# Performance work log

Measured on AMD Instinct MI355X. Metric: run time of the kernel, lower is better.

Reference implementation:

```python
import jax, jax.numpy as jnp
import numpy as np

D_MODEL = 1024
D_FF = 4096
N_EXPERTS = 8
TOP_K = 2
B, S = 4, 2048


def setup_inputs() -> dict:
    key = jax.random.key(0)
    ks = jax.random.split(key, 6)
    x = jax.random.normal(ks[0], (B, S, D_MODEL), dtype=jnp.float32)
    # router gate: nn.Linear(d_model, num_experts, bias=False), weight [E, D]
    gate_w = jax.random.normal(ks[1], (N_EXPERTS, D_MODEL), dtype=jnp.float32) * 0.01
    # expert MLPs, xavier-uniform init
    lim1 = float(np.sqrt(6.0 / (D_MODEL + D_FF)))
    W1 = jax.random.uniform(ks[2], (N_EXPERTS, D_FF, D_MODEL), minval=-lim1, maxval=lim1, dtype=jnp.float32)
    b1 = jnp.zeros((N_EXPERTS, D_FF), dtype=jnp.float32)
    W2 = jax.random.uniform(ks[3], (N_EXPERTS, D_MODEL, D_FF), minval=-lim1, maxval=lim1, dtype=jnp.float32)
    b2 = jnp.zeros((N_EXPERTS, D_MODEL), dtype=jnp.float32)
    return {"x": x, "gate_w": gate_w, "W1": W1, "b1": b1, "W2": W2, "b2": b2}


def reference(x, gate_w, W1, b1, W2, b2):
    Bb, Ss, D = x.shape
    xt = x.reshape(-1, D)                                  # [N, D]
    # --- router ---
    logits = xt @ gate_w.T                                 # [N, E]
    probs = jax.nn.softmax(logits, axis=-1)
    w_topk, idx = jax.lax.top_k(probs, TOP_K)              # [N, K]
    w_topk = w_topk / (jnp.sum(w_topk, axis=-1, keepdims=True) + 1e-9)
    # dense combine weights: zero for unselected experts    [N, E]
    comb = jnp.sum(jax.nn.one_hot(idx, N_EXPERTS, dtype=xt.dtype) * w_topk[..., None], axis=1)
    # --- experts (dense grouped GEMM over all experts) ---
    h = jnp.einsum('nd,efd->enf', xt, W1) + b1[:, None, :]  # [E, N, ff]
    h = jax.nn.relu(h)                                      # dropout=identity (eval)
    y = jnp.einsum('enf,edf->end', h, W2) + b2[:, None, :]  # [E, N, D]
    # --- weighted scatter/combine ---
    out = jnp.einsum('ne,end->nd', comb, y)                 # [N, D]
    return out.reshape(Bb, Ss, D)
```

## Files before the change

kernel.cpp:

```cpp
#include <hip/hip_runtime.h>
#include <hip/hip_bf16.h>
#include <stdint.h>

#define D_MODEL 1024
#define D_FF    4096
#define N_EXP   8
#define TOPK    2
#define NTOK    8192
#define NASSIGN (NTOK*TOPK)

#define BM 128
#define BN 128
#define BK 64
#define THREADS 256

typedef __bf16 bf16_t;
typedef __attribute__((ext_vector_type(8))) bf16_t bf16x8;
typedef __attribute__((ext_vector_type(4))) float f32x4;

__device__ __forceinline__ unsigned short f2bf(float f) {
    bf16_t b = (bf16_t)f;
    return __builtin_bit_cast(unsigned short, b);
}

__device__ __forceinline__ void gload_lds16(const void* g, void* l) {
    __builtin_amdgcn_global_load_lds(
        (const __attribute__((address_space(1))) void*)g,
        (__attribute__((address_space(3))) void*)l, 16, 0, 0);
}

__global__ void cvt_both_kernel(const float* __restrict__ W1, unsigned short* __restrict__ o1, int n1,
                                const float* __restrict__ W2, unsigned short* __restrict__ o2, int n2) {
    int stride = gridDim.x * blockDim.x;
    int q1 = n1 / 4, q2 = n2 / 4;
    for (int i = blockIdx.x * blockDim.x + threadIdx.x; i < q1 + q2; i += stride) {
        const float4* src; ushort4* dst; int k;
        if (i < q1) { src = (const float4*)W1; dst = (ushort4*)o1; k = i; }
        else        { src = (const float4*)W2; dst = (ushort4*)o2; k = i - q1; }
        float4 v = src[k];
        ushort4 o;
        o.x = f2bf(v.x); o.y = f2bf(v.y); o.z = f2bf(v.z); o.w = f2bf(v.w);
        dst[k] = o;
    }
}

__global__ __launch_bounds__(64) void router_kernel(
        const float* __restrict__ x, const float* __restrict__ gw,
        int* __restrict__ counts, int* __restrict__ ltok, float* __restrict__ lw,
        unsigned short* __restrict__ xb) {
    int n = blockIdx.x;
    int lane = threadIdx.x;
    const float* xr = x + (size_t)n * D_MODEL;
    unsigned short* xbr = xb + (size_t)n * D_MODEL;
    float acc[N_EXP];
    #pragma unroll
    for (int e = 0; e < N_EXP; e++) acc[e] = 0.f;
    #pragma unroll
    for (int i = 0; i < 4; i++) {
        int j = lane + i * 64;
        float4 v = ((const float4*)xr)[j];
        ushort4 o;
        o.x = f2bf(v.x); o.y = f2bf(v.y); o.z = f2bf(v.z); o.w = f2bf(v.w);
        ((ushort4*)xbr)[j] = o;
        int d = j * 4;
        #pragma unroll
        for (int e = 0; e < N_EXP; e++) {
            const float* g = gw + e * D_MODEL + d;
            acc[e] += v.x * g[0] + v.y * g[1] + v.z * g[2] + v.w * g[3];
        }
    }
    #pragma unroll
    for (int e = 0; e < N_EXP; e++) {
        #pragma unroll
        for (int off = 32; off > 0; off >>= 1)
            acc[e] += __shfl_down(acc[e], off);
    }
    if (lane == 0) {
        float mx = acc[0];
        #pragma unroll
        for (int e = 1; e < N_EXP; e++) mx = fmaxf(mx, acc[e]);
        float p[N_EXP];
        float s = 0.f;
        #pragma unroll
        for (int e = 0; e < N_EXP; e++) { p[e] = expf(acc[e] - mx); s += p[e]; }
        float inv = 1.f / s;
        #pragma unroll
        for (int e = 0; e < N_EXP; e++) p[e] *= inv;
        int i0 = 0;
        #pragma unroll
        for (int e = 1; e < N_EXP; e++) if (p[e] > p[i0]) i0 = e;
        int i1 = (i0 == 0) ? 1 : 0;
        #pragma unroll
        for (int e = 0; e < N_EXP; e++) if (e != i0 && p[e] > p[i1]) i1 = e;
        float s2 = p[i0] + p[i1] + 1e-9f;
        float w0 = p[i0] / s2, w1 = p[i1] / s2;
        int pos0 = atomicAdd(&counts[i0], 1);
        ltok[i0 * NTOK + pos0] = n; lw[i0 * NTOK + pos0] = w0;
        int pos1 = atomicAdd(&counts[i1], 1);
        ltok[i1 * NTOK + pos1] = n; lw[i1 * NTOK + pos1] = w1;
    }
}

__global__ void scan_kernel(const int* __restrict__ counts, int* __restrict__ offs) {
    if (threadIdx.x == 0 && blockIdx.x == 0) {
        int s = 0;
        for (int e = 0; e < N_EXP; e++) { offs[e] = s; s += counts[e]; }
    }
}


__global__ __launch_bounds__(THREADS, 3) void gemm1_kernel(
        const unsigned short* __restrict__ xb, const unsigned short* __restrict__ w1b,
        const float* __restrict__ b1,
        const int* __restrict__ counts, const int* __restrict__ offs,
        const int* __restrict__ ltok,
        unsigned short* __restrict__ hb) {
    const int NTM = NTOK / BM;
    int b = blockIdx.x;
    int e = b & 7;
    int idx = b >> 3;
    int nt = idx / NTM;
    int mt = idx % NTM;
    int cnt = counts[e];
    if (mt * BM >= cnt) return;

    __shared__ __align__(16) unsigned short As[BM * BK];
    __shared__ __align__(16) unsigned short Bs[BN * BK];

    int t = threadIdx.x;
    int lane = t & 63, w = t >> 6;
    int wr = w >> 1, wc = w & 1;

    int srow = t >> 3;
    int schunk = (t & 7) ^ (srow & 7);
    const unsigned short* aptr[4];
    const unsigned short* bptr[4];
    #pragma unroll
    for (int j = 0; j < 4; j++) {
        int rr = srow + j * 32;
        int slot = mt * BM + rr;
        int cs = slot < cnt ? slot : (cnt - 1);
        int tok = ltok[e * NTOK + cs];
        aptr[j] = xb + (size_t)tok * D_MODEL + schunk * 8;
        bptr[j] = w1b + ((size_t)e * D_FF + nt * BN + rr) * D_MODEL + schunk * 8;
    }
    char* As_b = (char*)As;
    char* Bs_b = (char*)Bs;

    int arow_base = wr * 64 + (lane & 15);
    int brow_base = wc * 64 + (lane & 15);
    int ch[2];
    #pragma unroll
    for (int ks = 0; ks < 2; ks++)
        ch[ks] = ((ks * 4 + (lane >> 4)) ^ (lane & 7)) << 4;

    f32x4 acc[4][4];
    #pragma unroll
    for (int m = 0; m < 4; m++)
        #pragma unroll
        for (int n = 0; n < 4; n++)
            acc[m][n] = (f32x4){0.f, 0.f, 0.f, 0.f};

    for (int k0 = 0; k0 < D_MODEL; k0 += BK) {
        #pragma unroll
        for (int j = 0; j < 4; j++) {
            gload_lds16(aptr[j] + k0, As_b + j * 4096 + t * 16);
            gload_lds16(bptr[j] + k0, Bs_b + j * 4096 + t * 16);
        }
        __syncthreads();
        bf16x8 af[2][4], bf[2][4];
        #pragma unroll
        for (int ks = 0; ks < 2; ks++) {
            #pragma unroll
            for (int m = 0; m < 4; m++)
                af[ks][m] = *(const bf16x8*)(As_b + (size_t)(arow_base + m * 16) * 128 + ch[ks]);
            #pragma unroll
            for (int n = 0; n < 4; n++)
                bf[ks][n] = *(const bf16x8*)(Bs_b + (size_t)(brow_base + n * 16) * 128 + ch[ks]);
        }
        #pragma unroll
        for (int ks = 0; ks < 2; ks++)
            #pragma unroll
            for (int m = 0; m < 4; m++)
                #pragma unroll
                for (int n = 0; n < 4; n++)
                    acc[m][n] = __builtin_amdgcn_mfma_f32_16x16x32_bf16(af[ks][m], bf[ks][n], acc[m][n], 0, 0, 0);
        __syncthreads();
    }

    int hbase = offs[e];
    float biasv[4];
    #pragma unroll
    for (int n = 0; n < 4; ++n)
        biasv[n] = b1[e * D_FF + nt * BN + wc * 64 + n * 16 + (lane & 15)];
    #pragma unroll
    for (int m = 0; m < 4; ++m) {
        int s0 = mt * BM + wr * 64 + m * 16 + (lane >> 4) * 4;
        #pragma unroll
        for (int rq = 0; rq < 4; ++rq) {
            int s = s0 + rq;
            if (s < cnt) {
                size_t rowoff = (size_t)(hbase + s) * D_FF + nt * BN + wc * 64 + (lane & 15);
                #pragma unroll
                for (int n = 0; n < 4; ++n) {
                    float v = fmaxf(acc[m][n][rq] + biasv[n], 0.f);
                    hb[rowoff + n * 16] = f2bf(v);
                }
            }
        }
    }
}

__global__ __launch_bounds__(THREADS, 3) void gemm2_kernel(
        const unsigned short* __restrict__ hb, const unsigned short* __restrict__ w2b,
        const float* __restrict__ b2,
        const int* __restrict__ counts, const int* __restrict__ offs,
        const int* __restrict__ ltok, const float* __restrict__ lw,
        float* __restrict__ out) {
    const int NTM = NTOK / BM;
    int b = blockIdx.x;
    int e = b & 7;
    int idx = b >> 3;
    int nt = idx / NTM;
    int mt = idx % NTM;
    int cnt = counts[e];
    if (mt * BM >= cnt) return;
    int hbase = offs[e];

    __shared__ __align__(16) unsigned short As[BM * BK];
    __shared__ __align__(16) unsigned short Bs[BN * BK];

    int t = threadIdx.x;
    int lane = t & 63, w = t >> 6;
    int wr = w >> 1, wc = w & 1;

    int srow = t >> 3;
    int schunk = (t & 7) ^ (srow & 7);
    const unsigned short* aptr[4];
    const unsigned short* bptr[4];
    #pragma unroll
    for (int j = 0; j < 4; j++) {
        int rr = srow + j * 32;
        int slot = mt * BM + rr;
        int cs = slot < cnt ? slot : (cnt - 1);
        aptr[j] = hb + (size_t)(hbase + cs) * D_FF + schunk * 8;
        bptr[j] = w2b + ((size_t)e * D_MODEL + nt * BN + rr) * D_FF + schunk * 8;
    }
    char* As_b = (char*)As;
    char* Bs_b = (char*)Bs;

    int arow_base = wr * 64 + (lane & 15);
    int brow_base = wc * 64 + (lane & 15);
    int ch[2];
    #pragma unroll
    for (int ks = 0; ks < 2; ks++)
        ch[ks] = ((ks * 4 + (lane >> 4)) ^ (lane & 7)) << 4;

    f32x4 acc[4][4];
    #pragma unroll
    for (int m = 0; m < 4; m++)
        #pragma unroll
        for (int n = 0; n < 4; n++)
            acc[m][n] = (f32x4){0.f, 0.f, 0.f, 0.f};

    for (int k0 = 0; k0 < D_FF; k0 += BK) {
        #pragma unroll
        for (int j = 0; j < 4; j++) {
            gload_lds16(aptr[j] + k0, As_b + j * 4096 + t * 16);
            gload_lds16(bptr[j] + k0, Bs_b + j * 4096 + t * 16);
        }
        __syncthreads();
        bf16x8 af[2][4], bf[2][4];
        #pragma unroll
        for (int ks = 0; ks < 2; ks++) {
            #pragma unroll
            for (int m = 0; m < 4; m++)
                af[ks][m] = *(const bf16x8*)(As_b + (size_t)(arow_base + m * 16) * 128 + ch[ks]);
            #pragma unroll
            for (int n = 0; n < 4; n++)
                bf[ks][n] = *(const bf16x8*)(Bs_b + (size_t)(brow_base + n * 16) * 128 + ch[ks]);
        }
        #pragma unroll
        for (int ks = 0; ks < 2; ks++)
            #pragma unroll
            for (int m = 0; m < 4; m++)
                #pragma unroll
                for (int n = 0; n < 4; n++)
                    acc[m][n] = __builtin_amdgcn_mfma_f32_16x16x32_bf16(af[ks][m], bf[ks][n], acc[m][n], 0, 0, 0);
        __syncthreads();
    }

    int lbase = e * NTOK;
    float biasv[4];
    #pragma unroll
    for (int n = 0; n < 4; ++n)
        biasv[n] = b2[e * D_MODEL + nt * BN + wc * 64 + n * 16 + (lane & 15)];
    #pragma unroll
    for (int m = 0; m < 4; ++m) {
        int s0 = mt * BM + wr * 64 + m * 16 + (lane >> 4) * 4;
        #pragma unroll
        for (int rq = 0; rq < 4; ++rq) {
            int s = s0 + rq;
            if (s >= cnt) continue;
            int tok = ltok[lbase + s];
            float wgt = lw[lbase + s];
            float* orow = out + (size_t)tok * D_MODEL + nt * BN + wc * 64 + (lane & 15);
            #pragma unroll
            for (int n = 0; n < 4; ++n)
                atomicAdd(orow + n * 16, wgt * (acc[m][n][rq] + biasv[n]));
        }
    }
}

extern "C" void kernel_launch(void* const* d_in, const int* in_sizes, int n_in,
                              void* d_out, int out_size, void* d_ws, size_t ws_size,
                              hipStream_t stream) {
    const float* x  = (const float*)d_in[0];
    const float* gw = (const float*)d_in[1];
    const float* W1 = (const float*)d_in[2];
    const float* b1 = (const float*)d_in[3];
    const float* W2 = (const float*)d_in[4];
    const float* b2 = (const float*)d_in[5];
    float* out = (float*)d_out;

    char* ws = (char*)d_ws;
    size_t off = 0;
    auto alloc = [&](size_t bytes) -> char* {
        char* p = ws + off;
        off += (bytes + 255) & ~(size_t)255;
        return p;
    };
    unsigned short* xb  = (unsigned short*)alloc((size_t)NTOK * D_MODEL * 2);
    unsigned short* w1b = (unsigned short*)alloc((size_t)N_EXP * D_FF * D_MODEL * 2);
    unsigned short* w2b = (unsigned short*)alloc((size_t)N_EXP * D_MODEL * D_FF * 2);
    unsigned short* hb  = (unsigned short*)alloc((size_t)NASSIGN * D_FF * 2);
    int*   counts = (int*)alloc(256);
    int*   offs   = (int*)alloc(256);
    int*   ltok   = (int*)alloc((size_t)N_EXP * NTOK * 4);
    float* lw     = (float*)alloc((size_t)N_EXP * NTOK * 4);

    hipMemsetAsync(out, 0, (size_t)out_size * 4, stream);
    hipMemsetAsync(counts, 0, 256, stream);
    cvt_both_kernel<<<8192, 256, 0, stream>>>(
        W1, w1b, N_EXP * D_FF * D_MODEL, W2, w2b, N_EXP * D_MODEL * D_FF);
    router_kernel<<<NTOK, 64, 0, stream>>>(x, gw, counts, ltok, lw, xb);
    scan_kernel<<<1, 64, 0, stream>>>(counts, offs);
    gemm1_kernel<<<N_EXP * (NTOK / BM) * (D_FF / BN), THREADS, 0, stream>>>(
        xb, w1b, b1, counts, offs, ltok, hb);
    gemm2_kernel<<<N_EXP * (NTOK / BM) * (D_MODEL / BN), THREADS, 0, stream>>>(
        hb, w2b, b2, counts, offs, ltok, lw, out);
}
```

Baseline: 681.1 us.

## Stage GEMM1 epilogue through LDS for 16-byte stores; widen weight conversion per thread

The GEMM1 epilogue now writes each wave's bf16 ReLU outputs into a padded LDS tile, reads them back as 8-element vectors, and issues coalesced 16-byte global stores to the hidden buffer. Before, each lane did scattered 2-byte stores. The weight conversion kernel now processes two float4 chunks per iteration with fewer blocks and uses 64-bit indices. The LDS staging reuses the A-tile buffer after the main loop and has no explicit barrier before it. That relies on the per-wave regions not overlapping data another wave still reads.

```diff
diff --git a/kernel.cpp b/kernel.cpp
--- a/kernel.cpp
+++ b/kernel.cpp
@@ -17,6 +17,7 @@
 typedef __bf16 bf16_t;
 typedef __attribute__((ext_vector_type(8))) bf16_t bf16x8;
 typedef __attribute__((ext_vector_type(4))) float f32x4;
+typedef __attribute__((ext_vector_type(8))) unsigned short u16x8;
 
 __device__ __forceinline__ unsigned short f2bf(float f) {
     bf16_t b = (bf16_t)f;
@@ -29,18 +30,21 @@
         (__attribute__((address_space(3))) void*)l, 16, 0, 0);
 }
 
-__global__ void cvt_both_kernel(const float* __restrict__ W1, unsigned short* __restrict__ o1, int n1,
-                                const float* __restrict__ W2, unsigned short* __restrict__ o2, int n2) {
-    int stride = gridDim.x * blockDim.x;
-    int q1 = n1 / 4, q2 = n2 / 4;
-    for (int i = blockIdx.x * blockDim.x + threadIdx.x; i < q1 + q2; i += stride) {
-        const float4* src; ushort4* dst; int k;
+__global__ void cvt_both_kernel(const float* __restrict__ W1, unsigned short* __restrict__ o1, long n1,
+                                const float* __restrict__ W2, unsigned short* __restrict__ o2, long n2) {
+    long stride = (long)gridDim.x * blockDim.x;
+    long q1 = n1 / 8, q2 = n2 / 8;
+    for (long i = (long)blockIdx.x * blockDim.x + threadIdx.x; i < q1 + q2; i += stride) {
+        const float4* src; ushort4* dst; long k;
         if (i < q1) { src = (const float4*)W1; dst = (ushort4*)o1; k = i; }
         else        { src = (const float4*)W2; dst = (ushort4*)o2; k = i - q1; }
-        float4 v = src[k];
-        ushort4 o;
-        o.x = f2bf(v.x); o.y = f2bf(v.y); o.z = f2bf(v.z); o.w = f2bf(v.w);
-        dst[k] = o;
+        float4 v0 = src[2 * k];
+        float4 v1 = src[2 * k + 1];
+        ushort4 a, b;
+        a.x = f2bf(v0.x); a.y = f2bf(v0.y); a.z = f2bf(v0.z); a.w = f2bf(v0.w);
+        b.x = f2bf(v1.x); b.y = f2bf(v1.y); b.z = f2bf(v1.z); b.w = f2bf(v1.w);
+        dst[2 * k] = a;
+        dst[2 * k + 1] = b;
     }
 }
 
@@ -193,19 +197,26 @@
     #pragma unroll
     for (int n = 0; n < 4; ++n)
         biasv[n] = b1[e * D_FF + nt * BN + wc * 64 + n * 16 + (lane & 15)];
+    unsigned short* Hs = (unsigned short*)(As_b) + w * 1216;
     #pragma unroll
     for (int m = 0; m < 4; ++m) {
-        int s0 = mt * BM + wr * 64 + m * 16 + (lane >> 4) * 4;
-        #pragma unroll
-        for (int rq = 0; rq < 4; ++rq) {
-            int s = s0 + rq;
+        #pragma unroll
+        for (int n = 0; n < 4; ++n) {
+            #pragma unroll
+            for (int rq = 0; rq < 4; ++rq) {
+                int lr = (lane >> 4) * 4 + rq;
+                int lc = n * 16 + (lane & 15);
+                float v = fmaxf(acc[m][n][rq] + biasv[n], 0.f);
+                Hs[lr * 72 + lc] = f2bf(v);
+            }
+        }
+        #pragma unroll
+        for (int half = 0; half < 2; ++half) {
+            int lr = half * 8 + (lane >> 3);
+            u16x8 vv = *(const u16x8*)(Hs + lr * 72 + (lane & 7) * 8);
+            int s = mt * BM + wr * 64 + m * 16 + lr;
             if (s < cnt) {
-                size_t rowoff = (size_t)(hbase + s) * D_FF + nt * BN + wc * 64 + (lane & 15);
-                #pragma unroll
-                for (int n = 0; n < 4; ++n) {
-                    float v = fmaxf(acc[m][n][rq] + biasv[n], 0.f);
-                    hb[rowoff + n * 16] = f2bf(v);
-                }
+                *(u16x8*)(hb + (size_t)(hbase + s) * D_FF + nt * BN + wc * 64 + (lane & 7) * 8) = vv;
             }
         }
     }
@@ -341,8 +352,8 @@
 
     hipMemsetAsync(out, 0, (size_t)out_size * 4, stream);
     hipMemsetAsync(counts, 0, 256, stream);
-    cvt_both_kernel<<<8192, 256, 0, stream>>>(
-        W1, w1b, N_EXP * D_FF * D_MODEL, W2, w2b, N_EXP * D_MODEL * D_FF);
+    cvt_both_kernel<<<2048, 256, 0, stream>>>(
+        W1, w1b, (long)N_EXP * D_FF * D_MODEL, W2, w2b, (long)N_EXP * D_MODEL * D_FF);
     router_kernel<<<NTOK, 64, 0, stream>>>(x, gw, counts, ltok, lw, xb);
     scan_kernel<<<1, 64, 0, stream>>>(counts, offs);
     gemm1_kernel<<<N_EXP * (NTOK / BM) * (D_FF / BN), THREADS, 0, stream>>>(
```

After: 674.0 us. Within noise of the previous version (-1.0%).
